# Kernel tuning notes

Hardware: AMD Instinct MI355X
Metric: run time of the kernel (lower is better)

Reference implementation:

```python
import jax, jax.numpy as jnp
import numpy as np

B, S, H, NH, I = 8, 1024, 1024, 16, 4096
HD = H // NH
EPS = 1e-6
NEG = -1e9


def _glorot(key, shape):
    lim = np.sqrt(6.0 / (shape[0] + shape[1]))
    return jax.random.uniform(key, shape, jnp.float32, -lim, lim)


def setup_inputs() -> dict:
    key = jax.random.key(0)
    ks = jax.random.split(key, 8)
    return {
        "inputs": jax.random.normal(ks[0], (B, S, H), jnp.float32),
        "inputs_mask": jnp.zeros((B, S), jnp.float32),  # 1.0 marks padding
        "attn_qkvw": _glorot(ks[1], (H, 3 * H)),
        "attn_qkvb": jnp.zeros((3 * H,), jnp.float32),
        "attn_ow": _glorot(ks[2], (H, H)),
        "attn_ob": jnp.zeros((H,), jnp.float32),
        "attn_nw": jnp.ones((H,), jnp.float32),
        "attn_nb": jnp.zeros((H,), jnp.float32),
        "inter_w": _glorot(ks[3], (H, I)),
        "inter_b": jnp.zeros((I,), jnp.float32),
        "output_w": _glorot(ks[4], (I, H)),
        "output_b": jnp.zeros((H,), jnp.float32),
        "ffn_nw": jnp.ones((H,), jnp.float32),
        "ffn_nb": jnp.zeros((H,), jnp.float32),
    }


def _layer_norm(x, g, b):
    m = jnp.mean(x, axis=-1, keepdims=True)
    v = jnp.mean(jnp.square(x - m), axis=-1, keepdims=True)
    return (x - m) * jax.lax.rsqrt(v + EPS) * g + b


def reference(inputs, inputs_mask, attn_qkvw, attn_qkvb, attn_ow, attn_ob,
              attn_nw, attn_nb, inter_w, inter_b, output_w, output_b,
              ffn_nw, ffn_nb):
    # ---- self-attention block (pre-LN) ----
    res = inputs
    x = _layer_norm(inputs, attn_nw, attn_nb)
    qkv = x @ attn_qkvw + attn_qkvb                      # [B,S,3H]
    q, k, v = jnp.split(qkv, 3, axis=-1)
    q = q.reshape(B, S, NH, HD)
    k = k.reshape(B, S, NH, HD)
    v = v.reshape(B, S, NH, HD)
    scale = 1.0 / np.sqrt(HD)
    scores = jnp.einsum("bqhd,bkhd->bhqk", q, k) * scale
    scores = scores + inputs_mask[:, None, None, :] * NEG
    probs = jax.nn.softmax(scores, axis=-1)
    ctx = jnp.einsum("bhqk,bkhd->bqhd", probs, v).reshape(B, S, H)
    attn_out = ctx @ attn_ow + attn_ob
    x = res + attn_out
    # ---- FFN block (pre-LN, ReLU) ----
    res2 = x
    y = _layer_norm(x, ffn_nw, ffn_nb)
    h = jax.nn.relu(y @ inter_w + inter_b)
    return res2 + h @ output_w + output_b
```

## Files before the change

kernel.cpp:

```cpp
#include <hip/hip_runtime.h>
#include <cstdint>
#include <cstddef>

typedef _Float16 f16;
typedef _Float16 half8 __attribute__((ext_vector_type(8)));
typedef _Float16 half4v __attribute__((ext_vector_type(4)));
typedef float floatx4 __attribute__((ext_vector_type(4)));

__device__ __forceinline__ floatx4 mfma16(half8 a, half8 b, floatx4 c) {
    return __builtin_amdgcn_mfma_f32_16x16x32_f16(a, b, c, 0, 0, 0);
}

__device__ __forceinline__ void async16(const f16* g, f16* l) {
    __builtin_amdgcn_global_load_lds(
        (const __attribute__((address_space(1))) unsigned int*)(uintptr_t)g,
        (__attribute__((address_space(3))) unsigned int*)(uintptr_t)l,
        16, 0, 0);
}

__global__ __launch_bounds__(256)
void ln_f16_kernel(const float* __restrict__ x, const float* __restrict__ g,
                   const float* __restrict__ be, f16* __restrict__ y)
{
    int row = blockIdx.x, t = threadIdx.x;
    const float* xr = x + (size_t)row * 1024;
    float4 v = *(const float4*)(xr + t * 4);
    float s1 = v.x + v.y + v.z + v.w;
    float s2 = v.x * v.x + v.y * v.y + v.z * v.z + v.w * v.w;
    #pragma unroll
    for (int off = 32; off >= 1; off >>= 1) {
        s1 += __shfl_xor(s1, off);
        s2 += __shfl_xor(s2, off);
    }
    __shared__ float r1[4], r2[4];
    if ((t & 63) == 0) { r1[t >> 6] = s1; r2[t >> 6] = s2; }
    __syncthreads();
    s1 = r1[0] + r1[1] + r1[2] + r1[3];
    s2 = r2[0] + r2[1] + r2[2] + r2[3];
    float mean = s1 * 0.0009765625f;
    float var  = s2 * 0.0009765625f - mean * mean;
    float rs = rsqrtf(var + 1e-6f);
    float4 gv = *(const float4*)(g + t * 4);
    float4 bv = *(const float4*)(be + t * 4);
    half4v o;
    o[0] = (f16)((v.x - mean) * rs * gv.x + bv.x);
    o[1] = (f16)((v.y - mean) * rs * gv.y + bv.y);
    o[2] = (f16)((v.z - mean) * rs * gv.z + bv.z);
    o[3] = (f16)((v.w - mean) * rs * gv.w + bv.w);
    *(half4v*)(y + (size_t)row * 1024 + t * 4) = o;
}

__global__ __launch_bounds__(256)
void transpose_f16_kernel(const float* __restrict__ W, f16* __restrict__ WT,
                          int R, int C)
{
    __shared__ float tile[32][33];
    int tx = threadIdx.x & 31, ty0 = threadIdx.x >> 5;
    int r0 = blockIdx.y * 32, c0 = blockIdx.x * 32;
    #pragma unroll
    for (int i = 0; i < 4; ++i)
        tile[ty0 + i * 8][tx] = W[(size_t)(r0 + ty0 + i * 8) * C + c0 + tx];
    __syncthreads();
    #pragma unroll
    for (int i = 0; i < 4; ++i)
        WT[(size_t)(c0 + ty0 + i * 8) * R + r0 + tx] = (f16)tile[tx][ty0 + i * 8];
}

template<int MODE>
__global__ __launch_bounds__(256, 2)
void gemm_kernel(const f16* __restrict__ A, const f16* __restrict__ BT,
                 const float* __restrict__ bias, const float* __restrict__ res,
                 float* __restrict__ Cf32, f16* __restrict__ Cf16,
                 f16* __restrict__ qb, f16* __restrict__ kb, f16* __restrict__ vb,
                 int M, int N, int K)
{
    __shared__ __align__(16) f16 As[128 * 64];
    __shared__ __align__(16) f16 Bs[128 * 64];
    int m0 = blockIdx.x * 128, n0 = blockIdx.y * 128;
    int t = threadIdx.x, lane = t & 63, wave = t >> 6;
    int quad = lane >> 4, l16 = lane & 15;
    int wm = (wave & 1) * 64, wn = (wave >> 1) * 64;
    int sw = l16 & 7;
    floatx4 acc[4][4] = {};

    for (int k0 = 0; k0 < K; k0 += 64) {
        __syncthreads();
        #pragma unroll
        for (int c = 0; c < 4; ++c) {
            int s = c * 256 + t;
            int row = s >> 3, phys = s & 7;
            int lg = phys ^ (row & 7);
            const f16* ga = A  + (size_t)(m0 + row) * K + k0 + lg * 8;
            const f16* gb = BT + (size_t)(n0 + row) * K + k0 + lg * 8;
            f16* la = As + (size_t)(c * 256 + (t & ~63)) * 8;
            f16* lb = Bs + (size_t)(c * 256 + (t & ~63)) * 8;
            async16(ga, la);
            async16(gb, lb);
        }
        __syncthreads();
        #pragma unroll
        for (int ks = 0; ks < 2; ++ks) {
            int ca = (ks * 4 + quad) ^ sw;
            half8 a[4], b[4];
            #pragma unroll
            for (int i = 0; i < 4; ++i) {
                a[i] = *(const half8*)(As + (wm + i * 16 + l16) * 64 + ca * 8);
                b[i] = *(const half8*)(Bs + (wn + i * 16 + l16) * 64 + ca * 8);
            }
            #pragma unroll
            for (int i = 0; i < 4; ++i)
                #pragma unroll
                for (int j = 0; j < 4; ++j)
                    acc[i][j] = mfma16(a[i], b[j], acc[i][j]);
        }
    }

    if (MODE == 2) {
        #pragma unroll
        for (int j = 0; j < 4; ++j) {
            int col = n0 + wn + j * 16 + l16;
            float bv = bias[col];
            int part = col >> 10;
            int h = (col >> 6) & 15;
            int d = col & 63;
            #pragma unroll
            for (int i = 0; i < 4; ++i) {
                int m = m0 + wm + i * 16 + quad * 4;
                int bb = m >> 10, s = m & 1023;
                size_t bh = (size_t)bb * 16 + h;
                if (part == 2) {
                    half4v pv;
                    #pragma unroll
                    for (int r = 0; r < 4; ++r) pv[r] = (f16)(acc[i][j][r] + bv);
                    *(half4v*)(vb + (bh * 64 + d) * 1024 + s) = pv;
                } else {
                    f16* dst = (part == 0 ? qb : kb) + (bh * 1024 + s) * 64 + d;
                    #pragma unroll
                    for (int r = 0; r < 4; ++r) dst[(size_t)r * 64] = (f16)(acc[i][j][r] + bv);
                }
            }
        }
    } else {
        #pragma unroll
        for (int j = 0; j < 4; ++j) {
            int col = n0 + wn + j * 16 + l16;
            float bv = bias[col];
            #pragma unroll
            for (int i = 0; i < 4; ++i) {
                int rowb = m0 + wm + i * 16 + quad * 4;
                #pragma unroll
                for (int r = 0; r < 4; ++r) {
                    float v = acc[i][j][r] + bv;
                    size_t idx = (size_t)(rowb + r) * N + col;
                    if (MODE == 1) Cf16[idx] = (f16)fmaxf(v, 0.f);
                    else           Cf32[idx] = v + res[idx];
                }
            }
        }
    }
}

__global__ __launch_bounds__(256)
void attn_kernel(const f16* __restrict__ qb, const f16* __restrict__ kb,
                 const f16* __restrict__ vb, const float* __restrict__ mask,
                 f16* __restrict__ ctx)
{
    const int S = 1024;
    int qt = blockIdx.x, h = blockIdx.y, b = blockIdx.z;
    size_t bh = (size_t)b * 16 + h;
    int t = threadIdx.x, lane = t & 63, wv = t >> 6;
    int quad = lane >> 4, l16 = lane & 15;
    int sw = l16 & 7;

    __shared__ __align__(16) f16 Ks[64 * 64];
    __shared__ __align__(16) f16 Vs[64 * 64];
    __shared__ __align__(16) f16 Ps[4][16 * 40];

    int q0 = qt * 64 + wv * 16;
    const f16* qrow = qb + (bh * 1024 + q0 + l16) * 64;
    half8 aq0 = *(const half8*)(qrow + quad * 8);
    half8 aq1 = *(const half8*)(qrow + 32 + quad * 8);

    floatx4 o[4] = {};
    float lsum[4] = {0.f, 0.f, 0.f, 0.f};
    const float scale = 0.125f;
    const float* mrow = mask + b * S;

    for (int kc = 0; kc < S; kc += 64) {
        __syncthreads();
        #pragma unroll
        for (int c = 0; c < 2; ++c) {
            int s = c * 256 + t;
            int row = s >> 3, phys = s & 7;
            int lg = phys ^ (row & 7);
            f16* lk = Ks + (size_t)(c * 256 + (t & ~63)) * 8;
            f16* lv = Vs + (size_t)(c * 256 + (t & ~63)) * 8;
            async16(kb + (bh * 1024 + kc + row) * 64 + lg * 8, lk);
            async16(vb + (bh * 64 + row) * 1024 + kc + lg * 8, lv);
        }
        __syncthreads();

        floatx4 sf[4];
        #pragma unroll
        for (int cg = 0; cg < 4; ++cg) {
            const f16* kr = Ks + (cg * 16 + l16) * 64;
            int c0 = quad ^ sw;
            half8 b0 = *(const half8*)(kr + c0 * 8);
            half8 b1 = *(const half8*)(kr + (c0 ^ 4) * 8);
            floatx4 z = {};
            sf[cg] = mfma16(aq1, b1, mfma16(aq0, b0, z));
        }
        #pragma unroll
        for (int cg = 0; cg < 4; ++cg) {
            float mk = mrow[kc + cg * 16 + l16] * (-1e9f);
            #pragma unroll
            for (int r = 0; r < 4; ++r) {
                float e = __expf(sf[cg][r] * scale + mk);
                lsum[r] += e;
                Ps[wv][(quad * 4 + r) * 40 + cg * 16 + l16] = (f16)e;
            }
        }
        half8 ap0 = *(const half8*)(Ps[wv] + l16 * 40 + quad * 8);
        half8 ap1 = *(const half8*)(Ps[wv] + l16 * 40 + 32 + quad * 8);
        #pragma unroll
        for (int td = 0; td < 4; ++td) {
            const f16* vr = Vs + (td * 16 + l16) * 64;
            int c0 = quad ^ sw;
            half8 bv0 = *(const half8*)(vr + c0 * 8);
            half8 bv1 = *(const half8*)(vr + (c0 ^ 4) * 8);
            o[td] = mfma16(ap0, bv0, o[td]);
            o[td] = mfma16(ap1, bv1, o[td]);
        }
    }

    #pragma unroll
    for (int r = 0; r < 4; ++r) {
        float s = lsum[r];
        s += __shfl_xor(s, 1); s += __shfl_xor(s, 2);
        s += __shfl_xor(s, 4); s += __shfl_xor(s, 8);
        lsum[r] = 1.f / s;
    }
    #pragma unroll
    for (int td = 0; td < 4; ++td)
        #pragma unroll
        for (int r = 0; r < 4; ++r)
            ctx[((size_t)b * 1024 + q0 + quad * 4 + r) * 1024 + h * 64 + td * 16 + l16]
                = (f16)(o[td][r] * lsum[r]);
}

extern "C" void kernel_launch(void* const* d_in, const int* in_sizes, int n_in,
                              void* d_out, int out_size, void* d_ws, size_t ws_size,
                              hipStream_t stream)
{
    const float* inputs = (const float*)d_in[0];
    const float* mask   = (const float*)d_in[1];
    const float* qkvw   = (const float*)d_in[2];
    const float* qkvb   = (const float*)d_in[3];
    const float* ow     = (const float*)d_in[4];
    const float* ob     = (const float*)d_in[5];
    const float* anw    = (const float*)d_in[6];
    const float* anb    = (const float*)d_in[7];
    const float* iw     = (const float*)d_in[8];
    const float* ib     = (const float*)d_in[9];
    const float* outw   = (const float*)d_in[10];
    const float* outb   = (const float*)d_in[11];
    const float* fnw    = (const float*)d_in[12];
    const float* fnb    = (const float*)d_in[13];
    float* out = (float*)d_out;

    const int M = 8192;
    uint8_t* ws = (uint8_t*)d_ws;
    f16* wT_qkv = (f16*)(ws + 0);
    f16* wT_o   = (f16*)(ws + 6291456);
    f16* wT_i   = (f16*)(ws + 8388608);
    f16* wT_out = (f16*)(ws + 16777216);
    f16* xln    = (f16*)(ws + 25165824);
    float* x1   = (float*)(ws + 41943040);
    f16* qbuf   = (f16*)(ws + 75497472);
    f16* kbuf   = (f16*)(ws + 92274688);
    f16* vbuf   = (f16*)(ws + 109051904);
    f16* ctx    = (f16*)(ws + 125829120);
    f16* hbuf   = (f16*)(ws + 75497472);

    transpose_f16_kernel<<<dim3(96, 32),  256, 0, stream>>>(qkvw, wT_qkv, 1024, 3072);
    transpose_f16_kernel<<<dim3(32, 32),  256, 0, stream>>>(ow,   wT_o,   1024, 1024);
    transpose_f16_kernel<<<dim3(128, 32), 256, 0, stream>>>(iw,   wT_i,   1024, 4096);
    transpose_f16_kernel<<<dim3(32, 128), 256, 0, stream>>>(outw, wT_out, 4096, 1024);

    ln_f16_kernel<<<8192, 256, 0, stream>>>(inputs, anw, anb, xln);

    gemm_kernel<2><<<dim3(64, 24), 256, 0, stream>>>(xln, wT_qkv, qkvb, nullptr,
        nullptr, nullptr, qbuf, kbuf, vbuf, M, 3072, 1024);

    attn_kernel<<<dim3(16, 16, 8), 256, 0, stream>>>(qbuf, kbuf, vbuf, mask, ctx);

    gemm_kernel<0><<<dim3(64, 8), 256, 0, stream>>>(ctx, wT_o, ob, inputs,
        x1, nullptr, nullptr, nullptr, nullptr, M, 1024, 1024);

    ln_f16_kernel<<<8192, 256, 0, stream>>>(x1, fnw, fnb, xln);

    gemm_kernel<1><<<dim3(64, 32), 256, 0, stream>>>(xln, wT_i, ib, nullptr,
        nullptr, hbuf, nullptr, nullptr, nullptr, M, 4096, 1024);

    gemm_kernel<0><<<dim3(64, 8), 256, 0, stream>>>(hbuf, wT_out, outb, x1,
        out, nullptr, nullptr, nullptr, nullptr, M, 1024, 4096);
}
```

Baseline: 489.8 us.

## Use 256x128 tiles with 32x32 MFMA for QKV and FFN-up GEMMs

Adds a separate GEMM kernel for the wide QKV and intermediate projections. It uses a 256x128 block tile, where each wave computes 64x128 with the 32x32x16 f16 MFMA instruction instead of 16x16x32. The larger tile and bigger MFMA raise arithmetic intensity per LDS load and halve the block count. In exchange it uses more LDS and accumulator registers (128 floats per thread), which may limit occupancy. The epilogue is rewritten for the 32x32 output layout, including the scattered Q/K/V writes.

```diff
diff --git a/kernel.cpp b/kernel.cpp
--- a/kernel.cpp
+++ b/kernel.cpp
@@ -6,9 +6,13 @@
 typedef _Float16 half8 __attribute__((ext_vector_type(8)));
 typedef _Float16 half4v __attribute__((ext_vector_type(4)));
 typedef float floatx4 __attribute__((ext_vector_type(4)));
+typedef float floatx16 __attribute__((ext_vector_type(16)));
 
 __device__ __forceinline__ floatx4 mfma16(half8 a, half8 b, floatx4 c) {
     return __builtin_amdgcn_mfma_f32_16x16x32_f16(a, b, c, 0, 0, 0);
+}
+__device__ __forceinline__ floatx16 mfma32(half8 a, half8 b, floatx16 c) {
+    return __builtin_amdgcn_mfma_f32_32x32x16_f16(a, b, c, 0, 0, 0);
 }
 
 __device__ __forceinline__ void async16(const f16* g, f16* l) {
@@ -66,13 +70,10 @@
         WT[(size_t)(c0 + ty0 + i * 8) * R + r0 + tx] = (f16)tile[tx][ty0 + i * 8];
 }
 
-template<int MODE>
 __global__ __launch_bounds__(256, 2)
 void gemm_kernel(const f16* __restrict__ A, const f16* __restrict__ BT,
                  const float* __restrict__ bias, const float* __restrict__ res,
-                 float* __restrict__ Cf32, f16* __restrict__ Cf16,
-                 f16* __restrict__ qb, f16* __restrict__ kb, f16* __restrict__ vb,
-                 int M, int N, int K)
+                 float* __restrict__ Cf32, int M, int N, int K)
 {
     __shared__ __align__(16) f16 As[128 * 64];
     __shared__ __align__(16) f16 Bs[128 * 64];
@@ -90,12 +91,10 @@
             int s = c * 256 + t;
             int row = s >> 3, phys = s & 7;
             int lg = phys ^ (row & 7);
-            const f16* ga = A  + (size_t)(m0 + row) * K + k0 + lg * 8;
-            const f16* gb = BT + (size_t)(n0 + row) * K + k0 + lg * 8;
-            f16* la = As + (size_t)(c * 256 + (t & ~63)) * 8;
-            f16* lb = Bs + (size_t)(c * 256 + (t & ~63)) * 8;
-            async16(ga, la);
-            async16(gb, lb);
+            async16(A  + (size_t)(m0 + row) * K + k0 + lg * 8,
+                    As + (size_t)(c * 256 + (t & ~63)) * 8);
+            async16(BT + (size_t)(n0 + row) * K + k0 + lg * 8,
+                    Bs + (size_t)(c * 256 + (t & ~63)) * 8);
         }
         __syncthreads();
         #pragma unroll
@@ -115,45 +114,118 @@
         }
     }
 
-    if (MODE == 2) {
-        #pragma unroll
-        for (int j = 0; j < 4; ++j) {
-            int col = n0 + wn + j * 16 + l16;
+    #pragma unroll
+    for (int j = 0; j < 4; ++j) {
+        int col = n0 + wn + j * 16 + l16;
+        float bv = bias[col];
+        #pragma unroll
+        for (int i = 0; i < 4; ++i) {
+            int rowb = m0 + wm + i * 16 + quad * 4;
+            #pragma unroll
+            for (int r = 0; r < 4; ++r) {
+                float v = acc[i][j][r] + bv;
+                size_t idx = (size_t)(rowb + r) * N + col;
+                Cf32[idx] = v + res[idx];
+            }
+        }
+    }
+}
+
+template<int MODE>
+__global__ __launch_bounds__(256, 2)
+void gemm_big_kernel(const f16* __restrict__ A, const f16* __restrict__ BT,
+                     const float* __restrict__ bias, f16* __restrict__ Cf16,
+                     f16* __restrict__ qb, f16* __restrict__ kb, f16* __restrict__ vb,
+                     int M, int N, int K)
+{
+    __shared__ __align__(16) f16 As[256 * 64];
+    __shared__ __align__(16) f16 Bs[128 * 64];
+    int m0 = blockIdx.x * 256, n0 = blockIdx.y * 128;
+    int t = threadIdx.x, lane = t & 63, wave = t >> 6;
+    int l32 = lane & 31, kg = lane >> 5;
+    int swz = l32 & 7;
+    floatx16 acc[2][4];
+    #pragma unroll
+    for (int mi = 0; mi < 2; ++mi)
+        #pragma unroll
+        for (int jn = 0; jn < 4; ++jn)
+            #pragma unroll
+            for (int r = 0; r < 16; ++r) acc[mi][jn][r] = 0.f;
+
+    for (int k0 = 0; k0 < K; k0 += 64) {
+        __syncthreads();
+        #pragma unroll
+        for (int c = 0; c < 8; ++c) {
+            int s = c * 256 + t;
+            int row = s >> 3, phys = s & 7;
+            int lg = phys ^ (row & 7);
+            async16(A + (size_t)(m0 + row) * K + k0 + lg * 8,
+                    As + (size_t)(c * 256 + (t & ~63)) * 8);
+        }
+        #pragma unroll
+        for (int c = 0; c < 4; ++c) {
+            int s = c * 256 + t;
+            int row = s >> 3, phys = s & 7;
+            int lg = phys ^ (row & 7);
+            async16(BT + (size_t)(n0 + row) * K + k0 + lg * 8,
+                    Bs + (size_t)(c * 256 + (t & ~63)) * 8);
+        }
+        __syncthreads();
+        #pragma unroll
+        for (int ss = 0; ss < 4; ++ss) {
+            int ca = (ss * 2 + kg) ^ swz;
+            half8 a[2], b[4];
+            #pragma unroll
+            for (int mi = 0; mi < 2; ++mi)
+                a[mi] = *(const half8*)(As + (wave * 64 + mi * 32 + l32) * 64 + ca * 8);
+            #pragma unroll
+            for (int jn = 0; jn < 4; ++jn)
+                b[jn] = *(const half8*)(Bs + (jn * 32 + l32) * 64 + ca * 8);
+            #pragma unroll
+            for (int mi = 0; mi < 2; ++mi)
+                #pragma unroll
+                for (int jn = 0; jn < 4; ++jn)
+                    acc[mi][jn] = mfma32(a[mi], b[jn], acc[mi][jn]);
+        }
+    }
+
+    #pragma unroll
+    for (int mi = 0; mi < 2; ++mi) {
+        int mbase = m0 + wave * 64 + mi * 32 + 4 * kg;
+        #pragma unroll
+        for (int jn = 0; jn < 4; ++jn) {
+            int col = n0 + jn * 32 + l32;
             float bv = bias[col];
-            int part = col >> 10;
-            int h = (col >> 6) & 15;
-            int d = col & 63;
-            #pragma unroll
-            for (int i = 0; i < 4; ++i) {
-                int m = m0 + wm + i * 16 + quad * 4;
-                int bb = m >> 10, s = m & 1023;
-                size_t bh = (size_t)bb * 16 + h;
+            if (MODE == 1) {
+                #pragma unroll
+                for (int reg = 0; reg < 16; ++reg) {
+                    int row = mbase + (reg & 3) + 8 * (reg >> 2);
+                    Cf16[(size_t)row * N + col] = (f16)fmaxf(acc[mi][jn][reg] + bv, 0.f);
+                }
+            } else {
+                int part = col >> 10;
+                int h = (col >> 6) & 15;
+                int d = col & 63;
                 if (part == 2) {
-                    half4v pv;
                     #pragma unroll
-                    for (int r = 0; r < 4; ++r) pv[r] = (f16)(acc[i][j][r] + bv);
-                    *(half4v*)(vb + (bh * 64 + d) * 1024 + s) = pv;
+                    for (int rb = 0; rb < 4; ++rb) {
+                        int m = mbase + 8 * rb;
+                        int bb = m >> 10, s = m & 1023;
+                        size_t bh = (size_t)bb * 16 + h;
+                        half4v pv;
+                        #pragma unroll
+                        for (int r = 0; r < 4; ++r) pv[r] = (f16)(acc[mi][jn][rb * 4 + r] + bv);
+                        *(half4v*)(vb + (bh * 64 + d) * 1024 + s) = pv;
+                    }
                 } else {
-                    f16* dst = (part == 0 ? qb : kb) + (bh * 1024 + s) * 64 + d;
+                    f16* dst0 = part == 0 ? qb : kb;
                     #pragma unroll
-                    for (int r = 0; r < 4; ++r) dst[(size_t)r * 64] = (f16)(acc[i][j][r] + bv);
-                }
-            }
-        }
-    } else {
-        #pragma unroll
-        for (int j = 0; j < 4; ++j) {
-            int col = n0 + wn + j * 16 + l16;
-            float bv = bias[col];
-            #pragma unroll
-            for (int i = 0; i < 4; ++i) {
-                int rowb = m0 + wm + i * 16 + quad * 4;
-                #pragma unroll
-                for (int r = 0; r < 4; ++r) {
-                    float v = acc[i][j][r] + bv;
-                    size_t idx = (size_t)(rowb + r) * N + col;
-                    if (MODE == 1) Cf16[idx] = (f16)fmaxf(v, 0.f);
-                    else           Cf32[idx] = v + res[idx];
+                    for (int reg = 0; reg < 16; ++reg) {
+                        int m = mbase + (reg & 3) + 8 * (reg >> 2);
+                        int bb = m >> 10, s = m & 1023;
+                        size_t bh = (size_t)bb * 16 + h;
+                        dst0[(bh * 1024 + s) * 64 + d] = (f16)(acc[mi][jn][reg] + bv);
+                    }
                 }
             }
         }
@@ -289,19 +361,19 @@
 
     ln_f16_kernel<<<8192, 256, 0, stream>>>(inputs, anw, anb, xln);
 
-    gemm_kernel<2><<<dim3(64, 24), 256, 0, stream>>>(xln, wT_qkv, qkvb, nullptr,
-        nullptr, nullptr, qbuf, kbuf, vbuf, M, 3072, 1024);
+    gemm_big_kernel<2><<<dim3(32, 24), 256, 0, stream>>>(xln, wT_qkv, qkvb,
+        nullptr, qbuf, kbuf, vbuf, M, 3072, 1024);
 
     attn_kernel<<<dim3(16, 16, 8), 256, 0, stream>>>(qbuf, kbuf, vbuf, mask, ctx);
 
-    gemm_kernel<0><<<dim3(64, 8), 256, 0, stream>>>(ctx, wT_o, ob, inputs,
-        x1, nullptr, nullptr, nullptr, nullptr, M, 1024, 1024);
+    gemm_kernel<<<dim3(64, 8), 256, 0, stream>>>(ctx, wT_o, ob, inputs,
+        x1, M, 1024, 1024);
 
     ln_f16_kernel<<<8192, 256, 0, stream>>>(x1, fnw, fnb, xln);
 
-    gemm_kernel<1><<<dim3(64, 32), 256, 0, stream>>>(xln, wT_i, ib, nullptr,
-        nullptr, hbuf, nullptr, nullptr, nullptr, M, 4096, 1024);
-
-    gemm_kernel<0><<<dim3(64, 8), 256, 0, stream>>>(hbuf, wT_out, outb, x1,
-        out, nullptr, nullptr, nullptr, nullptr, M, 1024, 4096);
-}
+    gemm_big_kernel<1><<<dim3(32, 32), 256, 0, stream>>>(xln, wT_i, ib,
+        hbuf, nullptr, nullptr, nullptr, M, 4096, 1024);
+
+    gemm_kernel<<<dim3(64, 8), 256, 0, stream>>>(hbuf, wT_out, outb, x1,
+        out, M, 1024, 4096);
+}
```

New measurement: 482.1 us. Within noise of the previous version (-1.6%).
